# Kernel tuning notes

Hardware: AMD Instinct MI355X
Metric: run time of the kernel (lower is better)

## Reference

```python
import jax, jax.numpy as jnp
import numpy as np

DIM = 256
HEADS = 4
HEAD_DIM = DIM // HEADS
SCALE = HEAD_DIM ** -0.5


def setup_inputs() -> dict:
    key = jax.random.key(0)
    ks = jax.random.split(key, 6)
    B, N, C = 4, 2048, DIM
    t2_grad = jax.random.normal(ks[0], (B, N, C), dtype=jnp.float32)
    t1 = jax.random.normal(ks[1], (B, N, C), dtype=jnp.float32)
    # Linear weights stored as (in, out) so y = x @ W
    Wq = jax.random.normal(ks[2], (C, C), dtype=jnp.float32) * (C ** -0.5)
    Wkv = jax.random.normal(ks[3], (C, 2 * C), dtype=jnp.float32) * (C ** -0.5)
    Wproj = jax.random.normal(ks[4], (C, C), dtype=jnp.float32) * (C ** -0.5)
    bproj = jax.random.normal(ks[5], (C,), dtype=jnp.float32) * 0.01
    gamma = jnp.zeros((1,), dtype=jnp.float32)
    return {"t2_grad": t2_grad, "t1": t1, "Wq": Wq, "Wkv": Wkv,
            "Wproj": Wproj, "bproj": bproj, "gamma": gamma}


def lam(x, gamma):
    # x: (B, H, N, d) -> channel attention over d
    B, H, N, d = x.shape
    xp = jnp.transpose(x, (0, 3, 1, 2))            # (B, d, H, N)
    flat = xp.reshape(B, d, H * N)                 # (B, d, H*N)
    energy = jnp.einsum('bdm,bem->bde', flat, flat)  # (B, d, d)
    # Original applies softmax to raw energy (energy_new is discarded)
    attention = jax.nn.softmax(energy, axis=-1)
    out = jnp.einsum('bde,bem->bdm', attention, flat).reshape(B, d, H, N)
    out = gamma[0] * out + xp
    return jnp.transpose(out, (0, 2, 3, 1))        # (B, H, N, d)


def reference(t2_grad, t1, Wq, Wkv, Wproj, bproj, gamma):
    B, N, C = t2_grad.shape
    H, d = HEADS, HEAD_DIM
    q = (t2_grad @ Wq).reshape(B, N, H, d).transpose(0, 2, 1, 3)      # (B,H,N,d)
    kv = (t1 @ Wkv).reshape(B, N, 2, H, d).transpose(2, 0, 3, 1, 4)   # (2,B,H,N,d)
    k, v = kv[0], kv[1]
    attn = jax.nn.softmax(jnp.einsum('bhnd,bhmd->bhnm', q, k) * SCALE, axis=-1)
    x_other = jnp.einsum('bhnm,bhmd->bhnd', attn, v)                  # (B,H,N,d)
    x_other = lam(x_other, gamma)
    x_other = x_other.transpose(0, 2, 1, 3).reshape(B, N, C) \
        + q.transpose(0, 2, 1, 3).reshape(B, N, C)
    x = t2_grad + x_other
    return x @ Wproj + bproj
```

## Files before the change

kernel.cpp:

```cpp
#include <hip/hip_runtime.h>
#include <hip/hip_bf16.h>


typedef __attribute__((ext_vector_type(8))) short short8_t;
typedef __attribute__((ext_vector_type(4))) float f32x4;
typedef __attribute__((ext_vector_type(2))) unsigned u32x2;

#define NSEQ 2048

static __device__ __forceinline__ short f2bf(float f) {
  union { float f; unsigned u; } v; v.f = f;
  unsigned u = v.u;
  unsigned r = (u + 0x7FFFu + ((u >> 16) & 1u)) >> 16;
  return (short)r;
}
static __device__ __forceinline__ float bf2f(short s) {
  union { unsigned u; float f; } v;
  v.u = ((unsigned)(unsigned short)s) << 16;
  return v.f;
}
static __device__ __forceinline__ unsigned bcu(float f) {
  return __builtin_bit_cast(unsigned, f);
}
static __device__ __forceinline__ unsigned pkbf(float lo, float hi) {
  return __builtin_amdgcn_perm(bcu(hi), bcu(lo), 0x07060302u);
}
static __device__ __forceinline__ short f2bf_hw(float f) {
  __hip_bfloat16 h = __float2bfloat16(f);
  return __builtin_bit_cast(short, h);
}
static __device__ __forceinline__ unsigned pk2bf_hw(float a, float b) {
  return ((unsigned)(unsigned short)__builtin_bit_cast(short, __float2bfloat16(b)) << 16) |
         (unsigned short)__builtin_bit_cast(short, __float2bfloat16(a));
}
static __device__ __forceinline__ f32x4 vmax4(f32x4 a, f32x4 b) {
  f32x4 r;
  r[0] = fmaxf(a[0], b[0]); r[1] = fmaxf(a[1], b[1]);
  r[2] = fmaxf(a[2], b[2]); r[3] = fmaxf(a[3], b[3]);
  return r;
}

static __device__ __forceinline__ void gload_lds16(const short* src, short* ldst) {
  __builtin_amdgcn_global_load_lds(
      (const __attribute__((address_space(1))) unsigned*)src,
      (__attribute__((address_space(3))) unsigned*)ldst, 16, 0, 0);
}

__global__ __launch_bounds__(256) void wconv(
    const float* __restrict__ Wq, const float* __restrict__ Wkv,
    const float* __restrict__ Wp, short* __restrict__ Wqt,
    short* __restrict__ Wkvt, short* __restrict__ Wpt) {
  int tid = blockIdx.x * 256 + threadIdx.x;
  if (tid < 65536) {
    int n = tid >> 8, k = tid & 255;
    Wqt[tid] = f2bf(Wq[k * 256 + n]);
  } else if (tid < 196608) {
    int i = tid - 65536;
    int n = i >> 8, k = i & 255;
    Wkvt[i] = f2bf(Wkv[k * 512 + n]);
  } else {
    int i = tid - 196608;
    int n = i >> 8, k = i & 255;
    Wpt[i] = f2bf(Wp[k * 256 + n]);
  }
}

__global__ __launch_bounds__(256) void gemm_qkv2(
    const float* __restrict__ t2, const float* __restrict__ t1,
    const short* __restrict__ Wqt, const short* __restrict__ Wkvt,
    short* __restrict__ Qb, short* __restrict__ Kb, short* __restrict__ Vtb) {
  __shared__ __align__(16) short ldsA[32 * 256];
  int tid = threadIdx.x;
  int m0 = blockIdx.x * 32;
  bool isQ = (blockIdx.y == 0);
  const float* A = isQ ? t2 : t1;

  const float* ap = A + (size_t)m0 * 256;
#pragma unroll
  for (int i = 0; i < 8; i++) {
    int idx = i * 256 + tid;
    int row = idx >> 6, c4 = idx & 63;
    f32x4 v = *(const f32x4*)(ap + (size_t)idx * 4);
    int ch8 = c4 >> 1, half = c4 & 1;
    int swz = ch8 ^ (row & 7);
    unsigned* dst = (unsigned*)&ldsA[row * 256 + swz * 8 + half * 4];
    dst[0] = pk2bf_hw(v[0], v[1]);
    dst[1] = pk2bf_hw(v[2], v[3]);
  }
  __syncthreads();

  int w = tid >> 6, l = tid & 63, lr = l & 15, lg = l >> 4;
  short8_t af[2][8];
#pragma unroll
  for (int mt = 0; mt < 2; mt++)
#pragma unroll
    for (int ks = 0; ks < 8; ks++)
      af[mt][ks] = *(const short8_t*)&ldsA[(mt * 16 + lr) * 256 +
                                           (((ks * 4 + lg) ^ (lr & 7)) * 8)];

  int nphase = isQ ? 1 : 2;
  for (int ph = 0; ph < nphase; ph++) {
    const short* Bt = isQ ? Wqt : (Wkvt + ph * 65536);
    f32x4 acc[2][4] = {};
#pragma unroll
    for (int ct = 0; ct < 4; ct++) {
      const short* br = Bt + (size_t)(w * 64 + ct * 16 + lr) * 256 + lg * 8;
      short8_t bfr[8];
#pragma unroll
      for (int ks = 0; ks < 8; ks++) bfr[ks] = *(const short8_t*)(br + ks * 32);
      if (ph == 0) {
#pragma unroll
        for (int ks = 0; ks < 8; ks++) {
          acc[0][ct] = __builtin_amdgcn_mfma_f32_16x16x32_bf16(af[0][ks], bfr[ks], acc[0][ct], 0, 0, 0);
          acc[1][ct] = __builtin_amdgcn_mfma_f32_16x16x32_bf16(af[1][ks], bfr[ks], acc[1][ct], 0, 0, 0);
        }
      } else {
#pragma unroll
        for (int ks = 0; ks < 8; ks++) {
          acc[0][ct] = __builtin_amdgcn_mfma_f32_16x16x32_bf16(bfr[ks], af[0][ks], acc[0][ct], 0, 0, 0);
          acc[1][ct] = __builtin_amdgcn_mfma_f32_16x16x32_bf16(bfr[ks], af[1][ks], acc[1][ct], 0, 0, 0);
        }
      }
    }
    if (ph == 0) {
      short* Ob = isQ ? Qb : Kb;
#pragma unroll
      for (int ct = 0; ct < 4; ct++) {
        int c = w * 64 + ct * 16 + lr;
        int h = c >> 6, dd = c & 63;
#pragma unroll
        for (int mt = 0; mt < 2; mt++)
#pragma unroll
          for (int r = 0; r < 4; r++) {
            int m = m0 + mt * 16 + lg * 4 + r;
            int bb = m >> 11, n = m & 2047;
            Ob[(size_t)(((bb << 2) + h) * NSEQ + n) * 64 + dd] =
                f2bf_hw(acc[mt][ct][r]);
          }
      }
    } else {
#pragma unroll
      for (int ct = 0; ct < 4; ct++) {
        int c = w * 64 + ct * 16 + lg * 4;
#pragma unroll
        for (int mt = 0; mt < 2; mt++) {
          int m = m0 + mt * 16 + lr;
          int bb = m >> 11, n = m & 2047;
#pragma unroll
          for (int r = 0; r < 4; r++) {
            int cc = c + r;
            int h = cc >> 6, dd = cc & 63;
            Vtb[(size_t)(((bb << 2) + h) * 64 + dd) * NSEQ + n] =
                f2bf_hw(acc[mt][ct][r]);
          }
        }
      }
    }
  }
}

template <int NS>
__global__ __launch_bounds__(256, 4) void flash_attn_split(
    const short* __restrict__ Qb, const short* __restrict__ Kb,
    const short* __restrict__ Vt, short* __restrict__ O0,
    short* __restrict__ O1, short* __restrict__ O2,
    short* __restrict__ O3, float* __restrict__ ML) {
  constexpr int KITER = 32 / NS;
  __shared__ __align__(16) short ldsK[2][4096];
  __shared__ __align__(16) short ldsV[4096];
  __shared__ __align__(16) short ldsP[4][2048];
  int tid = threadIdx.x;
  int w = tid >> 6, l = tid & 63, lr = l & 15, lg = l >> 4;
  int bh = blockIdx.y;
  int qt = blockIdx.x / NS, split = blockIdx.x % NS;
  int q0 = qt * 128 + w * 32;
  const short* qpA = Qb + ((size_t)bh * NSEQ + q0 + lr) * 64 + lg * 8;
  const short* qpB = qpA + 16 * 64;
  short8_t qfA0 = *(const short8_t*)qpA;
  short8_t qfA1 = *(const short8_t*)(qpA + 32);
  short8_t qfB0 = *(const short8_t*)qpB;
  short8_t qfB1 = *(const short8_t*)(qpB + 32);
  const short* kbase = Kb + (size_t)bh * NSEQ * 64;
  const short* vbase = Vt + (size_t)bh * 64 * NSEQ;

  int r0 = tid >> 3, ch0 = (tid & 7) ^ (r0 & 7);
  int kb0 = split * KITER;
  const short* ksrc = kbase + (size_t)kb0 * 4096 + (size_t)r0 * 64 + ch0 * 8;
  const short* vsrc = vbase + (size_t)r0 * NSEQ + kb0 * 64 + ch0 * 8;
  short* ldKw0 = &ldsK[0][0] + w * 512;
  short* ldKw1 = &ldsK[1][0] + w * 512;
  short* ldVw = &ldsV[0] + w * 512;

#define STAGE_K(dst_, it_)                                  \
  {                                                         \
    const short* s_ = ksrc + (size_t)(it_) * 4096;          \
    gload_lds16(s_, dst_);                                  \
    gload_lds16(s_ + 2048, (dst_) + 2048);                  \
  }
#define STAGE_V(it_)                                        \
  {                                                         \
    const short* s_ = vsrc + (size_t)(it_) * 64;            \
    gload_lds16(s_, ldVw);                                  \
    gload_lds16(s_ + 32 * NSEQ, ldVw + 2048);               \
  }

  f32x4 oA[4] = {}, oB[4] = {};
  float osumA = 0.f, osumB = 0.f, m2A = -1e30f, m2B = -1e30f;
  const float C = 0.125f * 1.44269504089f;

  int sw = lr & 7;
  int rdA = (lg ^ sw) * 8;
  int rdB = ((lg + 4) ^ sw) * 8;
  short* Pw = &ldsP[w][0];
  short* wrA = Pw + lr * 64 + (lg & 1) * 4;
  short* wrB = wrA + 16 * 64;
  int chhi = lg >> 1;
  const short* prA0 = Pw + lr * 64 + (lg ^ sw) * 8;
  const short* prA1 = Pw + lr * 64 + ((4 + lg) ^ sw) * 8;
  const short* prB0 = prA0 + 16 * 64;
  const short* prB1 = prA1 + 16 * 64;

  STAGE_K(ldKw0, 0);

  for (int i = 0; i < KITER; i++) {
    asm volatile("s_waitcnt vmcnt(0)" ::: "memory");
    __builtin_amdgcn_s_barrier();
    STAGE_V(i);
    if (i + 1 < KITER) {
      short* d_ = (i & 1) ? ldKw0 : ldKw1;
      STAGE_K(d_, i + 1);
    }
    const short* lK = (i & 1) ? &ldsK[1][0] : &ldsK[0][0];
    f32x4 sA[4], sB[4];
#pragma unroll
    for (int t = 0; t < 4; t++) {
      const short* kr = lK + (t * 16 + lr) * 64;
      short8_t kf0 = *(const short8_t*)(kr + rdA);
      short8_t kf1 = *(const short8_t*)(kr + rdB);
      f32x4 z = {0.f, 0.f, 0.f, 0.f};
      f32x4 zA = __builtin_amdgcn_mfma_f32_16x16x32_bf16(kf0, qfA0, z, 0, 0, 0);
      sA[t] = __builtin_amdgcn_mfma_f32_16x16x32_bf16(kf1, qfA1, zA, 0, 0, 0);
      f32x4 zB = __builtin_amdgcn_mfma_f32_16x16x32_bf16(kf0, qfB0, z, 0, 0, 0);
      sB[t] = __builtin_amdgcn_mfma_f32_16x16x32_bf16(kf1, qfB1, zB, 0, 0, 0);
    }
    f32x4 mA4 = vmax4(vmax4(sA[0], sA[1]), vmax4(sA[2], sA[3]));
    f32x4 mB4 = vmax4(vmax4(sB[0], sB[1]), vmax4(sB[2], sB[3]));
    float mxA = fmaxf(fmaxf(mA4[0], mA4[1]), fmaxf(mA4[2], mA4[3]));
    float mxB = fmaxf(fmaxf(mB4[0], mB4[1]), fmaxf(mB4[2], mB4[3]));
    mxA = fmaxf(mxA, __shfl_xor(mxA, 16));
    mxA = fmaxf(mxA, __shfl_xor(mxA, 32));
    mxB = fmaxf(mxB, __shfl_xor(mxB, 16));
    mxB = fmaxf(mxB, __shfl_xor(mxB, 32));
    mxA *= C;
    mxB *= C;
    float mnA = fmaxf(m2A, mxA), mnB = fmaxf(m2B, mxB);
    if (__any(fmaxf(mnA - m2A, mnB - m2B) > 8.f)) {
      float aA = __builtin_amdgcn_exp2f(m2A - mnA);
      float aB = __builtin_amdgcn_exp2f(m2B - mnB);
      m2A = mnA; m2B = mnB;
      osumA *= aA; osumB *= aB;
#pragma unroll
      for (int dt = 0; dt < 4; dt++) { oA[dt] *= aA; oB[dt] *= aB; }
    }
    float psA = 0.f, psB = 0.f;
#pragma unroll
    for (int t = 0; t < 4; t++) {
      float a0 = __builtin_amdgcn_exp2f(__builtin_fmaf(sA[t][0], C, -m2A));
      float a1 = __builtin_amdgcn_exp2f(__builtin_fmaf(sA[t][1], C, -m2A));
      float a2 = __builtin_amdgcn_exp2f(__builtin_fmaf(sA[t][2], C, -m2A));
      float a3 = __builtin_amdgcn_exp2f(__builtin_fmaf(sA[t][3], C, -m2A));
      psA += (a0 + a1) + (a2 + a3);
      u32x2 ua = {pkbf(a0, a1), pkbf(a2, a3)};
      *(u32x2*)(wrA + ((2 * t + chhi) ^ sw) * 8) = ua;
      float b0 = __builtin_amdgcn_exp2f(__builtin_fmaf(sB[t][0], C, -m2B));
      float b1 = __builtin_amdgcn_exp2f(__builtin_fmaf(sB[t][1], C, -m2B));
      float b2 = __builtin_amdgcn_exp2f(__builtin_fmaf(sB[t][2], C, -m2B));
      float b3 = __builtin_amdgcn_exp2f(__builtin_fmaf(sB[t][3], C, -m2B));
      psB += (b0 + b1) + (b2 + b3);
      u32x2 ub = {pkbf(b0, b1), pkbf(b2, b3)};
      *(u32x2*)(wrB + ((2 * t + chhi) ^ sw) * 8) = ub;
    }
    osumA += psA;
    osumB += psB;
    short8_t pA0 = *(const short8_t*)prA0;
    short8_t pA1 = *(const short8_t*)prA1;
    short8_t pB0 = *(const short8_t*)prB0;
    short8_t pB1 = *(const short8_t*)prB1;
    if (i + 1 < KITER)
      asm volatile("s_waitcnt vmcnt(2)" ::: "memory");
    else
      asm volatile("s_waitcnt vmcnt(0)" ::: "memory");
    __builtin_amdgcn_s_barrier();
#pragma unroll
    for (int dt = 0; dt < 4; dt++) {
      const short* vr = &ldsV[0] + (dt * 16 + lr) * 64;
      short8_t vf0 = *(const short8_t*)(vr + rdA);
      short8_t vf1 = *(const short8_t*)(vr + rdB);
      oA[dt] = __builtin_amdgcn_mfma_f32_16x16x32_bf16(vf0, pA0, oA[dt], 0, 0, 0);
      oA[dt] = __builtin_amdgcn_mfma_f32_16x16x32_bf16(vf1, pA1, oA[dt], 0, 0, 0);
      oB[dt] = __builtin_amdgcn_mfma_f32_16x16x32_bf16(vf0, pB0, oB[dt], 0, 0, 0);
      oB[dt] = __builtin_amdgcn_mfma_f32_16x16x32_bf16(vf1, pB1, oB[dt], 0, 0, 0);
    }
  }
#undef STAGE_K
#undef STAGE_V
  osumA += __shfl_xor(osumA, 16);
  osumA += __shfl_xor(osumA, 32);
  osumB += __shfl_xor(osumB, 16);
  osumB += __shfl_xor(osumB, 32);
  float invA = __builtin_amdgcn_rcpf(osumA);
  float invB = __builtin_amdgcn_rcpf(osumB);
  short* op = (split == 0) ? O0 : (split == 1) ? O1 : (split == 2) ? O2 : O3;
#pragma unroll
  for (int dt = 0; dt < 4; dt++)
#pragma unroll
    for (int r = 0; r < 4; r++) {
      size_t drow = ((size_t)bh * 64 + dt * 16 + lg * 4 + r) * NSEQ;
      op[drow + q0 + lr] = f2bf_hw(oA[dt][r] * invA);
      op[drow + q0 + 16 + lr] = f2bf_hw(oB[dt][r] * invB);
    }
  if (lg == 0) {
    float2 vA = {m2A, osumA};
    float2 vB = {m2B, osumB};
    *(float2*)&ML[((size_t)bh * NSEQ + q0 + lr) * 8 + split * 2] = vA;
    *(float2*)&ML[((size_t)bh * NSEQ + q0 + 16 + lr) * 8 + split * 2] = vB;
  }
}

template <int NS>
__global__ __launch_bounds__(256) void combine_xf(
    const short* __restrict__ O0, const short* __restrict__ O1,
    const short* __restrict__ O2, const short* __restrict__ O3,
    const float* __restrict__ ML, const float* __restrict__ gamma,
    const float* __restrict__ t2, const short* __restrict__ Qb,
    short* __restrict__ AOb, float* __restrict__ partials,
    short* __restrict__ Xf) {
  __shared__ __align__(16) short tileT[64][128];
  __shared__ f32x4 wcol[128];
  int tid = threadIdx.x;
  int b = blockIdx.y, kc = blockIdx.x;
  int h = kc >> 4, n0 = (kc & 15) * 128;
  int bh = (b << 2) + h;
  float g = gamma[0];
  if (tid < 128) {
    const float* ml = ML + ((size_t)bh * NSEQ + n0 + tid) * 8;
    f32x4 a = *(const f32x4*)ml;
    f32x4 c;
    if (NS == 2) {
      float M = fmaxf(a[0], a[2]);
      float w0 = a[1] * __builtin_amdgcn_exp2f(a[0] - M);
      float w1 = a[3] * __builtin_amdgcn_exp2f(a[2] - M);
      float iv = __builtin_amdgcn_rcpf(w0 + w1);
      c[0] = w0 * iv; c[1] = w1 * iv; c[2] = 0.f; c[3] = 0.f;
    } else {
      f32x4 bq = *(const f32x4*)(ml + 4);
      float M = fmaxf(fmaxf(a[0], a[2]), fmaxf(bq[0], bq[2]));
      float w0 = a[1] * __builtin_amdgcn_exp2f(a[0] - M);
      float w1 = a[3] * __builtin_amdgcn_exp2f(a[2] - M);
      float w2 = bq[1] * __builtin_amdgcn_exp2f(bq[0] - M);
      float w3 = bq[3] * __builtin_amdgcn_exp2f(bq[2] - M);
      float iv = __builtin_amdgcn_rcpf(w0 + w1 + w2 + w3);
      c[0] = w0 * iv; c[1] = w1 * iv; c[2] = w2 * iv; c[3] = w3 * iv;
    }
    wcol[tid] = c;
  }
  __syncthreads();
  {
    int row = tid >> 2, c0 = (tid & 3) * 32;
    size_t gbase = ((size_t)bh * 64 + row) * NSEQ + n0 + c0;
    int rsw = row & 15;
    short* trow = &tileT[row][0];
#pragma unroll
    for (int i = 0; i < 4; i++) {
      short8_t v0 = *(const short8_t*)(O0 + gbase + i * 8);
      short8_t v1 = *(const short8_t*)(O1 + gbase + i * 8);
      short8_t v2{}, v3{};
      if (NS == 4) {
        v2 = *(const short8_t*)(O2 + gbase + i * 8);
        v3 = *(const short8_t*)(O3 + gbase + i * 8);
      }
      short8_t comb;
#pragma unroll
      for (int j = 0; j < 8; j++) {
        f32x4 c = wcol[c0 + i * 8 + j];
        float val = bf2f(v0[j]) * c[0] + bf2f(v1[j]) * c[1];
        if (NS == 4) val += bf2f(v2[j]) * c[2] + bf2f(v3[j]) * c[3];
        comb[j] = f2bf_hw(val);
      }
      if (g != 0.f) *(short8_t*)(AOb + gbase + i * 8) = comb;
      int ch = ((c0 >> 3) + i) ^ rsw;
      *(short8_t*)(trow + ch * 8) = comb;
    }
  }
  __syncthreads();
  if (g == 0.f) {
    int nc = tid >> 1, half = tid & 1;
    int n = n0 + nc;
    int cidx = nc >> 3, jj = nc & 7;
    const float* t2p = t2 + ((size_t)b * NSEQ + n) * 256 + h * 64 + half * 32;
    const short* qp = Qb + ((size_t)bh * NSEQ + n) * 64 + half * 32;
    short* xfp = Xf + ((size_t)b * NSEQ + n) * 256 + h * 64 + half * 32;
#pragma unroll
    for (int i = 0; i < 4; i++) {
      int ddb = half * 32 + i * 8;
      f32x4 ta = *(const f32x4*)(t2p + i * 8);
      f32x4 tb = *(const f32x4*)(t2p + i * 8 + 4);
      short8_t q8 = *(const short8_t*)(qp + i * 8);
      short8_t r;
#pragma unroll
      for (int j = 0; j < 8; j++) {
        int dd = ddb + j;
        short xv = tileT[dd][((cidx ^ (dd & 15)) * 8) + jj];
        float t = (j < 4) ? ta[j] : tb[j - 4];
        r[j] = f2bf_hw(t + bf2f(xv) + bf2f(q8[j]));
      }
      *(short8_t*)(xfp + i * 8) = r;
    }
    return;
  }
  int w = tid >> 6, lr = tid & 15, lg = (tid & 63) >> 4;
  f32x4 acc[4] = {};
#pragma unroll
  for (int ks = 0; ks < 4; ks++) {
    short8_t af = *(const short8_t*)&tileT[w * 16 + lr][((ks * 4 + lg) ^ lr) * 8];
#pragma unroll
    for (int e = 0; e < 4; e++) {
      short8_t bf = *(const short8_t*)&tileT[e * 16 + lr][((ks * 4 + lg) ^ lr) * 8];
      acc[e] = __builtin_amdgcn_mfma_f32_16x16x32_bf16(af, bf, acc[e], 0, 0, 0);
    }
  }
  float* dst = partials + ((size_t)b * 64 + kc) * 4096;
#pragma unroll
  for (int e = 0; e < 4; e++)
#pragma unroll
    for (int r = 0; r < 4; r++)
      dst[(w * 16 + lg * 4 + r) * 64 + e * 16 + lr] = acc[e][r];
}

__global__ __launch_bounds__(64) void energy_reduce_softmax(
    const float* __restrict__ partials, const float* __restrict__ gamma,
    float* __restrict__ attnc) {
  if (gamma[0] == 0.f) return;
  int row = blockIdx.x;
  int b = row >> 6, d = row & 63;
  int e = threadIdx.x;
  const float* src = partials + (size_t)b * 64 * 4096 + d * 64 + e;
  float s = 0.f;
#pragma unroll 8
  for (int kc = 0; kc < 64; kc++) s += src[(size_t)kc * 4096];
  float mx = s;
#pragma unroll
  for (int x = 1; x < 64; x <<= 1) mx = fmaxf(mx, __shfl_xor(mx, x, 64));
  float ev = __expf(s - mx);
  float sum = ev;
#pragma unroll
  for (int x = 1; x < 64; x <<= 1) sum += __shfl_xor(sum, x, 64);
  attnc[row * 64 + e] = ev / sum;
}

__global__ __launch_bounds__(256) void assemble_x(
    const short* __restrict__ AOb, const float* __restrict__ attnc,
    const float* __restrict__ t2, const short* __restrict__ Qb,
    const float* __restrict__ gamma, short* __restrict__ Xf) {
  float g = gamma[0];
  if (g == 0.f) return;
  __shared__ f32x4 At4[1024];
  int b = blockIdx.y, tid = threadIdx.x;
  const f32x4* ac = (const f32x4*)(attnc + (size_t)b * 4096);
#pragma unroll
  for (int i = 0; i < 4; i++) At4[i * 256 + tid] = ac[i * 256 + tid];
  __syncthreads();
  int rowb = blockIdx.x * 256 + tid;
  int h = rowb >> 11, n = rowb & 2047;
  const short* xop = AOb + ((size_t)((b << 2) + h) * 64) * NSEQ + n;
  f32x4 xv[16];
#pragma unroll
  for (int i = 0; i < 16; i++) {
    f32x4 t;
    t[0] = bf2f(xop[(size_t)(4 * i + 0) * NSEQ]);
    t[1] = bf2f(xop[(size_t)(4 * i + 1) * NSEQ]);
    t[2] = bf2f(xop[(size_t)(4 * i + 2) * NSEQ]);
    t[3] = bf2f(xop[(size_t)(4 * i + 3) * NSEQ]);
    xv[i] = t;
  }
  const short* qp = Qb + ((size_t)b * 8192 + rowb) * 64;
  const float* t2p = t2 + ((size_t)b * 2048 + n) * 256 + h * 64;
  short* xfp = Xf + ((size_t)b * 2048 + n) * 256 + h * 64;
#pragma unroll
  for (int dd = 0; dd < 64; dd++) {
    f32x4 a = {0.f, 0.f, 0.f, 0.f};
#pragma unroll
    for (int j = 0; j < 16; j++) a += At4[dd * 16 + j] * xv[j];
    float o = (a[0] + a[1] + a[2] + a[3]) * g;
    float val = t2p[dd] + o + xv[dd >> 2][dd & 3] + bf2f(qp[dd]);
    xfp[dd] = f2bf(val);
  }
}

__global__ __launch_bounds__(256) void gemm_proj(
    const short* __restrict__ Xf, const short* __restrict__ Wpt,
    const float* __restrict__ bias, float* __restrict__ out) {
  int w = threadIdx.x >> 6, l = threadIdx.x & 63, lr = l & 15, lg = l >> 4;
  int m0 = blockIdx.x * 64 + w * 16;
  int n0 = blockIdx.y * 64;
  short8_t af[8];
  const short* ar = Xf + (size_t)(m0 + lr) * 256 + lg * 8;
#pragma unroll
  for (int ks = 0; ks < 8; ks++) af[ks] = *(const short8_t*)(ar + ks * 32);
  for (int ct = 0; ct < 4; ct++) {
    f32x4 acc = {0.f, 0.f, 0.f, 0.f};
    const short* br = Wpt + (size_t)(n0 + ct * 16 + lr) * 256 + lg * 8;
#pragma unroll
    for (int ks = 0; ks < 8; ks++) {
      short8_t bf = *(const short8_t*)(br + ks * 32);
      acc = __builtin_amdgcn_mfma_f32_16x16x32_bf16(af[ks], bf, acc, 0, 0, 0);
    }
    int c = n0 + ct * 16 + lr;
    float bc = bias[c];
#pragma unroll
    for (int r = 0; r < 4; r++) {
      int m = m0 + lg * 4 + r;
      out[(size_t)m * 256 + c] = acc[r] + bc;
    }
  }
}

extern "C" void kernel_launch(void* const* d_in, const int* in_sizes, int n_in,
                              void* d_out, int out_size, void* d_ws, size_t ws_size,
                              hipStream_t stream) {
  const float* t2 = (const float*)d_in[0];
  const float* t1 = (const float*)d_in[1];
  const float* Wq = (const float*)d_in[2];
  const float* Wkv = (const float*)d_in[3];
  const float* Wp = (const float*)d_in[4];
  const float* bproj = (const float*)d_in[5];
  const float* gamma = (const float*)d_in[6];
  float* out = (float*)d_out;
  char* ws = (char*)d_ws;

  const size_t MB = 1024ull * 1024ull;
  short* Qb = (short*)(ws + 0);
  short* Kb = (short*)(ws + 4 * MB);
  float* partials = (float*)(ws + 4 * MB);
  short* Vt = (short*)(ws + 8 * MB);
  short* AOb = (short*)(ws + 8 * MB);
  short* Xf = (short*)(ws + 12 * MB);
  short* O0 = (short*)(ws + 16 * MB);
  short* O1 = (short*)(ws + 20 * MB);
  short* Wqt = (short*)(ws + 24 * MB);
  short* Wkvt = (short*)(ws + 24 * MB + 128 * 1024);
  short* Wpt = (short*)(ws + 24 * MB + 384 * 1024);
  float* attnc = (float*)(ws + 24 * MB + 512 * 1024);
  float* ML = (float*)(ws + 24 * MB + 576 * 1024);
  short* O2 = (short*)(ws + 26 * MB);
  short* O3 = (short*)(ws + 30 * MB);

  bool big = ws_size >= 34 * MB;

  wconv<<<1024, 256, 0, stream>>>(Wq, Wkv, Wp, Wqt, Wkvt, Wpt);
  gemm_qkv2<<<dim3(256, 2), 256, 0, stream>>>(t2, t1, Wqt, Wkvt, Qb, Kb, Vt);
  if (big) {
    flash_attn_split<4><<<dim3(64, 16), 256, 0, stream>>>(Qb, Kb, Vt, O0, O1,
                                                          O2, O3, ML);
    combine_xf<4><<<dim3(64, 4), 256, 0, stream>>>(
        O0, O1, O2, O3, ML, gamma, t2, Qb, AOb, partials, Xf);
  } else {
    flash_attn_split<2><<<dim3(32, 16), 256, 0, stream>>>(Qb, Kb, Vt, O0, O1,
                                                          O1, O1, ML);
    combine_xf<2><<<dim3(64, 4), 256, 0, stream>>>(
        O0, O1, O1, O1, ML, gamma, t2, Qb, AOb, partials, Xf);
  }
  energy_reduce_softmax<<<256, 64, 0, stream>>>(partials, gamma, attnc);
  assemble_x<<<dim3(32, 4), 256, 0, stream>>>(AOb, attnc, t2, Qb, gamma, Xf);
  gemm_proj<<<dim3(128, 4), 256, 0, stream>>>(Xf, Wpt, bproj, out);
}
```

Before: 80.04 us.

## Split QKV gemm into three block rows, add MFMA priority, retile proj gemm

Splits the K/V projection phases into separate grid rows, so the QKV gemm launches 3x256 blocks and per-block work is balanced instead of K/V blocks doing two phases. Adds s_setprio around the MFMA sections in flash attention to favour matrix issue across waves. Changes the combine kernel's global read pattern so 16 threads cover a row contiguously. Rewrites gemm_proj to stage a 16-row A tile in LDS via direct loads, with each block covering all 256 output columns. The trade-off is that t1 is now re-read and re-converted by two blocks for K and V, and the proj gemm has more blocks each loading the full weight matrix.

```diff
diff --git a/kernel.cpp b/kernel.cpp
--- a/kernel.cpp
+++ b/kernel.cpp
@@ -65,15 +65,15 @@
   }
 }
 
-__global__ __launch_bounds__(256) void gemm_qkv2(
+__global__ __launch_bounds__(256) void gemm_qkv3(
     const float* __restrict__ t2, const float* __restrict__ t1,
     const short* __restrict__ Wqt, const short* __restrict__ Wkvt,
     short* __restrict__ Qb, short* __restrict__ Kb, short* __restrict__ Vtb) {
   __shared__ __align__(16) short ldsA[32 * 256];
   int tid = threadIdx.x;
   int m0 = blockIdx.x * 32;
-  bool isQ = (blockIdx.y == 0);
-  const float* A = isQ ? t2 : t1;
+  int y = blockIdx.y;
+  const float* A = (y == 0) ? t2 : t1;
 
   const float* ap = A + (size_t)m0 * 256;
 #pragma unroll
@@ -98,61 +98,58 @@
       af[mt][ks] = *(const short8_t*)&ldsA[(mt * 16 + lr) * 256 +
                                            (((ks * 4 + lg) ^ (lr & 7)) * 8)];
 
-  int nphase = isQ ? 1 : 2;
-  for (int ph = 0; ph < nphase; ph++) {
-    const short* Bt = isQ ? Wqt : (Wkvt + ph * 65536);
-    f32x4 acc[2][4] = {};
-#pragma unroll
-    for (int ct = 0; ct < 4; ct++) {
-      const short* br = Bt + (size_t)(w * 64 + ct * 16 + lr) * 256 + lg * 8;
-      short8_t bfr[8];
-#pragma unroll
-      for (int ks = 0; ks < 8; ks++) bfr[ks] = *(const short8_t*)(br + ks * 32);
-      if (ph == 0) {
-#pragma unroll
-        for (int ks = 0; ks < 8; ks++) {
-          acc[0][ct] = __builtin_amdgcn_mfma_f32_16x16x32_bf16(af[0][ks], bfr[ks], acc[0][ct], 0, 0, 0);
-          acc[1][ct] = __builtin_amdgcn_mfma_f32_16x16x32_bf16(af[1][ks], bfr[ks], acc[1][ct], 0, 0, 0);
-        }
-      } else {
-#pragma unroll
-        for (int ks = 0; ks < 8; ks++) {
-          acc[0][ct] = __builtin_amdgcn_mfma_f32_16x16x32_bf16(bfr[ks], af[0][ks], acc[0][ct], 0, 0, 0);
-          acc[1][ct] = __builtin_amdgcn_mfma_f32_16x16x32_bf16(bfr[ks], af[1][ks], acc[1][ct], 0, 0, 0);
-        }
-      }
-    }
-    if (ph == 0) {
-      short* Ob = isQ ? Qb : Kb;
-#pragma unroll
-      for (int ct = 0; ct < 4; ct++) {
-        int c = w * 64 + ct * 16 + lr;
-        int h = c >> 6, dd = c & 63;
-#pragma unroll
-        for (int mt = 0; mt < 2; mt++)
-#pragma unroll
-          for (int r = 0; r < 4; r++) {
-            int m = m0 + mt * 16 + lg * 4 + r;
-            int bb = m >> 11, n = m & 2047;
-            Ob[(size_t)(((bb << 2) + h) * NSEQ + n) * 64 + dd] =
-                f2bf_hw(acc[mt][ct][r]);
-          }
+  const short* Bt = (y == 0) ? Wqt : (y == 1 ? Wkvt : Wkvt + 65536);
+  f32x4 acc[2][4] = {};
+#pragma unroll
+  for (int ct = 0; ct < 4; ct++) {
+    const short* br = Bt + (size_t)(w * 64 + ct * 16 + lr) * 256 + lg * 8;
+    short8_t bfr[8];
+#pragma unroll
+    for (int ks = 0; ks < 8; ks++) bfr[ks] = *(const short8_t*)(br + ks * 32);
+    if (y < 2) {
+#pragma unroll
+      for (int ks = 0; ks < 8; ks++) {
+        acc[0][ct] = __builtin_amdgcn_mfma_f32_16x16x32_bf16(af[0][ks], bfr[ks], acc[0][ct], 0, 0, 0);
+        acc[1][ct] = __builtin_amdgcn_mfma_f32_16x16x32_bf16(af[1][ks], bfr[ks], acc[1][ct], 0, 0, 0);
       }
     } else {
 #pragma unroll
-      for (int ct = 0; ct < 4; ct++) {
-        int c = w * 64 + ct * 16 + lg * 4;
-#pragma unroll
-        for (int mt = 0; mt < 2; mt++) {
-          int m = m0 + mt * 16 + lr;
+      for (int ks = 0; ks < 8; ks++) {
+        acc[0][ct] = __builtin_amdgcn_mfma_f32_16x16x32_bf16(bfr[ks], af[0][ks], acc[0][ct], 0, 0, 0);
+        acc[1][ct] = __builtin_amdgcn_mfma_f32_16x16x32_bf16(bfr[ks], af[1][ks], acc[1][ct], 0, 0, 0);
+      }
+    }
+  }
+  if (y < 2) {
+    short* Ob = (y == 0) ? Qb : Kb;
+#pragma unroll
+    for (int ct = 0; ct < 4; ct++) {
+      int c = w * 64 + ct * 16 + lr;
+      int h = c >> 6, dd = c & 63;
+#pragma unroll
+      for (int mt = 0; mt < 2; mt++)
+#pragma unroll
+        for (int r = 0; r < 4; r++) {
+          int m = m0 + mt * 16 + lg * 4 + r;
           int bb = m >> 11, n = m & 2047;
-#pragma unroll
-          for (int r = 0; r < 4; r++) {
-            int cc = c + r;
-            int h = cc >> 6, dd = cc & 63;
-            Vtb[(size_t)(((bb << 2) + h) * 64 + dd) * NSEQ + n] =
-                f2bf_hw(acc[mt][ct][r]);
-          }
+          Ob[(size_t)(((bb << 2) + h) * NSEQ + n) * 64 + dd] =
+              f2bf_hw(acc[mt][ct][r]);
+        }
+    }
+  } else {
+#pragma unroll
+    for (int ct = 0; ct < 4; ct++) {
+      int c = w * 64 + ct * 16 + lg * 4;
+#pragma unroll
+      for (int mt = 0; mt < 2; mt++) {
+        int m = m0 + mt * 16 + lr;
+        int bb = m >> 11, n = m & 2047;
+#pragma unroll
+        for (int r = 0; r < 4; r++) {
+          int cc = c + r;
+          int h = cc >> 6, dd = cc & 63;
+          Vtb[(size_t)(((bb << 2) + h) * 64 + dd) * NSEQ + n] =
+              f2bf_hw(acc[mt][ct][r]);
         }
       }
     }
@@ -232,6 +229,7 @@
     }
     const short* lK = (i & 1) ? &ldsK[1][0] : &ldsK[0][0];
     f32x4 sA[4], sB[4];
+    __builtin_amdgcn_s_setprio(1);
 #pragma unroll
     for (int t = 0; t < 4; t++) {
       const short* kr = lK + (t * 16 + lr) * 64;
@@ -243,6 +241,7 @@
       f32x4 zB = __builtin_amdgcn_mfma_f32_16x16x32_bf16(kf0, qfB0, z, 0, 0, 0);
       sB[t] = __builtin_amdgcn_mfma_f32_16x16x32_bf16(kf1, qfB1, zB, 0, 0, 0);
     }
+    __builtin_amdgcn_s_setprio(0);
     f32x4 mA4 = vmax4(vmax4(sA[0], sA[1]), vmax4(sA[2], sA[3]));
     f32x4 mB4 = vmax4(vmax4(sB[0], sB[1]), vmax4(sB[2], sB[3]));
     float mxA = fmaxf(fmaxf(mA4[0], mA4[1]), fmaxf(mA4[2], mA4[3]));
@@ -291,6 +290,7 @@
     else
       asm volatile("s_waitcnt vmcnt(0)" ::: "memory");
     __builtin_amdgcn_s_barrier();
+    __builtin_amdgcn_s_setprio(1);
 #pragma unroll
     for (int dt = 0; dt < 4; dt++) {
       const short* vr = &ldsV[0] + (dt * 16 + lr) * 64;
@@ -301,6 +301,7 @@
       oB[dt] = __builtin_amdgcn_mfma_f32_16x16x32_bf16(vf0, pB0, oB[dt], 0, 0, 0);
       oB[dt] = __builtin_amdgcn_mfma_f32_16x16x32_bf16(vf1, pB1, oB[dt], 0, 0, 0);
     }
+    __builtin_amdgcn_s_setprio(0);
   }
 #undef STAGE_K
 #undef STAGE_V
@@ -366,30 +367,29 @@
   }
   __syncthreads();
   {
-    int row = tid >> 2, c0 = (tid & 3) * 32;
-    size_t gbase = ((size_t)bh * 64 + row) * NSEQ + n0 + c0;
-    int rsw = row & 15;
-    short* trow = &tileT[row][0];
+    int chunk = tid & 15;
+    int rw = tid >> 4;
 #pragma unroll
     for (int i = 0; i < 4; i++) {
-      short8_t v0 = *(const short8_t*)(O0 + gbase + i * 8);
-      short8_t v1 = *(const short8_t*)(O1 + gbase + i * 8);
+      int row = rw + 16 * i;
+      size_t gbase = ((size_t)bh * 64 + row) * NSEQ + n0 + chunk * 8;
+      short8_t v0 = *(const short8_t*)(O0 + gbase);
+      short8_t v1 = *(const short8_t*)(O1 + gbase);
       short8_t v2{}, v3{};
       if (NS == 4) {
-        v2 = *(const short8_t*)(O2 + gbase + i * 8);
-        v3 = *(const short8_t*)(O3 + gbase + i * 8);
+        v2 = *(const short8_t*)(O2 + gbase);
+        v3 = *(const short8_t*)(O3 + gbase);
       }
       short8_t comb;
 #pragma unroll
       for (int j = 0; j < 8; j++) {
-        f32x4 c = wcol[c0 + i * 8 + j];
+        f32x4 c = wcol[chunk * 8 + j];
         float val = bf2f(v0[j]) * c[0] + bf2f(v1[j]) * c[1];
         if (NS == 4) val += bf2f(v2[j]) * c[2] + bf2f(v3[j]) * c[3];
         comb[j] = f2bf_hw(val);
       }
-      if (g != 0.f) *(short8_t*)(AOb + gbase + i * 8) = comb;
-      int ch = ((c0 >> 3) + i) ^ rsw;
-      *(short8_t*)(trow + ch * 8) = comb;
+      if (g != 0.f) *(short8_t*)(AOb + gbase) = comb;
+      *(short8_t*)&tileT[row][(chunk ^ (row & 15)) * 8] = comb;
     }
   }
   __syncthreads();
@@ -500,27 +500,43 @@
 __global__ __launch_bounds__(256) void gemm_proj(
     const short* __restrict__ Xf, const short* __restrict__ Wpt,
     const float* __restrict__ bias, float* __restrict__ out) {
-  int w = threadIdx.x >> 6, l = threadIdx.x & 63, lr = l & 15, lg = l >> 4;
-  int m0 = blockIdx.x * 64 + w * 16;
-  int n0 = blockIdx.y * 64;
+  __shared__ __align__(16) short ldsA[16 * 256];
+  int tid = threadIdx.x;
+  int w = tid >> 6, l = tid & 63, lr = l & 15, lg = l >> 4;
+  int m0 = blockIdx.x * 16;
+#pragma unroll
+  for (int i = 0; i < 2; i++) {
+    int c = w * 128 + i * 64 + l;
+    int row = c >> 5, ch = c & 31;
+    int chs = (ch & 24) | ((ch & 7) ^ (row & 7));
+    gload_lds16(Xf + (size_t)(m0 + row) * 256 + chs * 8,
+                &ldsA[(w * 128 + i * 64) * 8]);
+  }
+  asm volatile("s_waitcnt vmcnt(0)" ::: "memory");
+  __syncthreads();
   short8_t af[8];
-  const short* ar = Xf + (size_t)(m0 + lr) * 256 + lg * 8;
-#pragma unroll
-  for (int ks = 0; ks < 8; ks++) af[ks] = *(const short8_t*)(ar + ks * 32);
+#pragma unroll
+  for (int ks = 0; ks < 8; ks++)
+    af[ks] = *(const short8_t*)&ldsA[lr * 256 + (((ks * 4 + lg) ^ (lr & 7)) * 8)];
+  f32x4 acc[4] = {};
+#pragma unroll
   for (int ct = 0; ct < 4; ct++) {
-    f32x4 acc = {0.f, 0.f, 0.f, 0.f};
-    const short* br = Wpt + (size_t)(n0 + ct * 16 + lr) * 256 + lg * 8;
-#pragma unroll
-    for (int ks = 0; ks < 8; ks++) {
-      short8_t bf = *(const short8_t*)(br + ks * 32);
-      acc = __builtin_amdgcn_mfma_f32_16x16x32_bf16(af[ks], bf, acc, 0, 0, 0);
-    }
-    int c = n0 + ct * 16 + lr;
+    const short* br = Wpt + (size_t)(w * 64 + ct * 16 + lr) * 256 + lg * 8;
+    short8_t bfr[8];
+#pragma unroll
+    for (int ks = 0; ks < 8; ks++) bfr[ks] = *(const short8_t*)(br + ks * 32);
+#pragma unroll
+    for (int ks = 0; ks < 8; ks++)
+      acc[ct] = __builtin_amdgcn_mfma_f32_16x16x32_bf16(af[ks], bfr[ks], acc[ct], 0, 0, 0);
+  }
+#pragma unroll
+  for (int ct = 0; ct < 4; ct++) {
+    int c = w * 64 + ct * 16 + lr;
     float bc = bias[c];
 #pragma unroll
     for (int r = 0; r < 4; r++) {
       int m = m0 + lg * 4 + r;
-      out[(size_t)m * 256 + c] = acc[r] + bc;
+      out[(size_t)m * 256 + c] = acc[ct][r] + bc;
     }
   }
 }
@@ -558,7 +574,7 @@
   bool big = ws_size >= 34 * MB;
 
   wconv<<<1024, 256, 0, stream>>>(Wq, Wkv, Wp, Wqt, Wkvt, Wpt);
-  gemm_qkv2<<<dim3(256, 2), 256, 0, stream>>>(t2, t1, Wqt, Wkvt, Qb, Kb, Vt);
+  gemm_qkv3<<<dim3(256, 3), 256, 0, stream>>>(t2, t1, Wqt, Wkvt, Qb, Kb, Vt);
   if (big) {
     flash_attn_split<4><<<dim3(64, 16), 256, 0, stream>>>(Qb, Kb, Vt, O0, O1,
                                                           O2, O3, ML);
@@ -572,5 +588,5 @@
   }
   energy_reduce_softmax<<<256, 64, 0, stream>>>(partials, gamma, attnc);
   assemble_x<<<dim3(32, 4), 256, 0, stream>>>(AOb, attnc, t2, Qb, gamma, Xf);
-  gemm_proj<<<dim3(128, 4), 256, 0, stream>>>(Xf, Wpt, bproj, out);
-}
+  gemm_proj<<<512, 256, 0, stream>>>(Xf, Wpt, bproj, out);
+}
```

New measurement: 78.56 us. Within noise of the previous version (-1.8%).
